# Optimization experiments

Hardware: AMD Instinct MI355X
Metric: run time of the kernel (lower is better)

Reference implementation:

```python
import jax, jax.numpy as jnp
import numpy as np

N, E, X_DIM, EA_DIM, HID, NL, NC, NGRAPH = 50000, 800000, 64, 16, 64, 3, 10, 64
BN_EPS = 1e-5
STD_EPS = 1e-5


def setup_inputs() -> dict:
    key = jax.random.key(0)
    ks = jax.random.split(key, 24)
    w = lambda k, sh: (jax.random.normal(k, sh, jnp.float32) * 0.05)
    inp = {
        'x': jax.random.normal(ks[0], (N, X_DIM), jnp.float32),
        'edge_index': jax.random.randint(ks[1], (2, E), 0, N),
        'batch': jnp.sort(jax.random.randint(ks[2], (N,), 0, NGRAPH)),
        'edge_attr': jax.random.normal(ks[3], (E, EA_DIM), jnp.float32),
        # node / edge encoders
        'node_w': w(ks[4], (X_DIM, HID)), 'node_b': jnp.zeros((HID,), jnp.float32),
        'edge_w': w(ks[5], (EA_DIM, HID)), 'edge_b': jnp.zeros((HID,), jnp.float32),
        # per-layer PNA post_nn Linear(12*3*HID -> HID) and BatchNorm
        'conv_w': w(ks[6], (NL, 12 * 3 * HID, HID)), 'conv_b': jnp.zeros((NL, HID), jnp.float32),
        'bn_g': jnp.ones((NL, HID), jnp.float32), 'bn_b': jnp.zeros((NL, HID), jnp.float32),
        # fc_out: HID -> HID/2 -> HID/4 -> NC
        'fc1_w': w(ks[7], (HID, HID // 2)), 'fc1_b': jnp.zeros((HID // 2,), jnp.float32),
        'fc2_w': w(ks[8], (HID // 2, HID // 4)), 'fc2_b': jnp.zeros((HID // 4,), jnp.float32),
        'fc3_w': w(ks[9], (HID // 4, NC)), 'fc3_b': jnp.zeros((NC,), jnp.float32),
    }
    return inp


def _pna_layer(x, src, dst, ea, deg, degc, log_deg, avg_log, w, b):
    # message: concat([x_i, x_j, edge_attr]) with x_i = x[dst], x_j = x[src]  -> [E, 3H]
    h = jnp.concatenate([x[dst], x[src], ea], axis=-1)
    inv = (1.0 / degc)[:, None]
    s1 = jax.ops.segment_sum(h, dst, num_segments=N)
    mean = s1 * inv
    mean_sq = jax.ops.segment_sum(h * h, dst, num_segments=N) * inv
    std = jnp.sqrt(jax.nn.relu(mean_sq - mean * mean) + STD_EPS)
    has = (deg > 0)[:, None]
    mx = jax.ops.segment_max(h, dst, num_segments=N)
    mx = jnp.where(has, mx, 0.0)
    mn = -jax.ops.segment_max(-h, dst, num_segments=N)
    mn = jnp.where(has, mn, 0.0)
    out = jnp.concatenate([mean, mn, mx, std], axis=-1)  # [N, 4*3H]
    amp = (log_deg / avg_log)[:, None]
    att = (avg_log / log_deg)[:, None]
    out = jnp.concatenate([out, out * amp, out * att], axis=-1)  # [N, 12*3H]
    return out @ w + b


def reference(x, edge_index, batch, edge_attr, node_w, node_b, edge_w, edge_b,
              conv_w, conv_b, bn_g, bn_b, fc1_w, fc1_b, fc2_w, fc2_b, fc3_w, fc3_b):
    src, dst = edge_index[0], edge_index[1]
    x = x @ node_w + node_b
    ea = edge_attr @ edge_w + edge_b
    deg = jax.ops.segment_sum(jnp.ones((E,), jnp.float32), dst, num_segments=N)
    degc = jnp.maximum(deg, 1.0)
    log_deg = jnp.log(degc + 1.0)
    # avg of log(deg+1) over nodes (equivalent to the histogram-based avg_deg['log'])
    avg_log = jnp.mean(jnp.log(deg + 1.0))
    for i in range(NL):
        h = _pna_layer(x, src, dst, ea, deg, degc, log_deg, avg_log, conv_w[i], conv_b[i])
        mu = jnp.mean(h, axis=0)
        var = jnp.mean((h - mu) ** 2, axis=0)  # biased var, as torch BN training mode
        h = (h - mu) * jax.lax.rsqrt(var + BN_EPS) * bn_g[i] + bn_b[i]
        x = jax.nn.relu(h) + x  # dropout is identity in eval
    # global mean pool over graphs
    gsum = jax.ops.segment_sum(x, batch, num_segments=NGRAPH)
    gcnt = jnp.maximum(jax.ops.segment_sum(jnp.ones((N,), jnp.float32), batch, num_segments=NGRAPH), 1.0)
    g = gsum / gcnt[:, None]
    g = jax.nn.relu(g @ fc1_w + fc1_b)
    g = jax.nn.relu(g @ fc2_w + fc2_b)
    return g @ fc3_w + fc3_b
```

## Files before the change

### kernel.cpp

```cpp
#include <hip/hip_runtime.h>
#include <math.h>

#define N_NODES 50000
#define N_EDGES 800000
#define NGRAPH  64
#define KEFF    576

typedef short bf16x8 __attribute__((ext_vector_type(8)));
typedef float f32x4  __attribute__((ext_vector_type(4)));
typedef float f32x16 __attribute__((ext_vector_type(16)));
typedef unsigned int u32;
typedef unsigned int u32x4 __attribute__((ext_vector_type(4)));

__device__ inline unsigned short f2bf_rne(float f) {
  unsigned u = __float_as_uint(f);
  unsigned r = u + 0x7FFFu + ((u >> 16) & 1u);
  return (unsigned short)(r >> 16);
}
__device__ inline float bf2f(unsigned short h) {
  return __uint_as_float(((unsigned)h) << 16);
}

__device__ inline u32 cvtpk_bf16(float a, float b) {
  u32 r;
  asm("v_cvt_pk_bf16_f32 %0, %1, %2" : "=v"(r) : "v"(a), "v"(b));
  return r;
}

__device__ inline void split2(float a, float b, u32& ph, u32& pl) {
  ph = cvtpk_bf16(a, b);
  float ha = __uint_as_float(ph << 16);
  float hb = __uint_as_float(ph & 0xFFFF0000u);
  pl = cvtpk_bf16(a - ha, b - hb);
}

__device__ inline bf16x8 pack_bf(u32 w0, u32 w1, u32 w2, u32 w3) {
  u32x4 t;
  t.x = w0; t.y = w1; t.z = w2; t.w = w3;
  return __builtin_bit_cast(bf16x8, t);
}


__global__ __launch_bounds__(256) void zero_kernel(
    int* __restrict__ cnt, float* __restrict__ gsum,
    double* __restrict__ bnacc, double* __restrict__ avgacc)
{
  int i = blockIdx.x * 256 + threadIdx.x;
  if (i < N_NODES) { cnt[i] = 0; return; }
  int j = i - N_NODES;
  if (j < NGRAPH * 64) { gsum[j] = 0.f; return; }
  int k = j - NGRAPH * 64;
  if (k < 3 * 128) { bnacc[k] = 0.0; return; }
  if (k == 3 * 128) *avgacc = 0.0;
}

__global__ __launch_bounds__(256) void node_enc_kernel(
    const float* __restrict__ xin, const float* __restrict__ nw,
    const float* __restrict__ nb, float* __restrict__ x)
{
  __shared__ float xs[256];
  int tid = threadIdx.x;
  int base = blockIdx.x * 256;
  xs[tid] = xin[base + tid];
  __syncthreads();
  int r = tid >> 6, j = tid & 63;
  float acc = nb[j];
#pragma unroll
  for (int t = 0; t < 64; t++) acc = fmaf(xs[r * 64 + t], nw[t * 64 + j], acc);
  x[base + tid] = acc;
}

__global__ void count_kernel(const int* __restrict__ dst, int* __restrict__ cnt,
                             int* __restrict__ rank)
{
  int e = blockIdx.x * 256 + threadIdx.x;
  rank[e] = atomicAdd(&cnt[dst[e]], 1);
}

__global__ __launch_bounds__(256) void scan_a_kernel(
    const int* __restrict__ cnt, int* __restrict__ bsum)
{
  __shared__ int s[256];
  int i = blockIdx.x * 256 + threadIdx.x;
  s[threadIdx.x] = (i < N_NODES) ? cnt[i] : 0;
  __syncthreads();
  for (int off = 128; off > 0; off >>= 1) {
    if (threadIdx.x < off) s[threadIdx.x] += s[threadIdx.x + off];
    __syncthreads();
  }
  if (threadIdx.x == 0) bsum[blockIdx.x] = s[0];
}

__global__ __launch_bounds__(256) void scan_b_kernel(
    const int* __restrict__ bsum, int* __restrict__ boff)
{
  __shared__ int s[256];
  int tid = threadIdx.x;
  int v = (tid < 196) ? bsum[tid] : 0;
  s[tid] = v;
  __syncthreads();
  for (int off = 1; off < 256; off <<= 1) {
    int t = (tid >= off) ? s[tid - off] : 0;
    __syncthreads();
    s[tid] += t;
    __syncthreads();
  }
  boff[tid] = s[tid] - v;
}

__global__ __launch_bounds__(256) void scan_c_kernel(
    const int* __restrict__ cnt, const int* __restrict__ boff,
    int* __restrict__ row_ptr)
{
  __shared__ int s[256];
  int tid = threadIdx.x;
  int i = blockIdx.x * 256 + tid;
  int v = (i < N_NODES) ? cnt[i] : 0;
  s[tid] = v;
  __syncthreads();
  for (int off = 1; off < 256; off <<= 1) {
    int t = (tid >= off) ? s[tid - off] : 0;
    __syncthreads();
    s[tid] += t;
    __syncthreads();
  }
  int incl = s[tid];
  int base = boff[blockIdx.x];
  if (i < N_NODES) row_ptr[i] = base + incl - v;
  if (i == N_NODES - 1) row_ptr[N_NODES] = base + incl;
}

__global__ void fill_kernel(const int* __restrict__ src, const int* __restrict__ dst,
                            const int* __restrict__ rank, const int* __restrict__ row_ptr,
                            int2* __restrict__ edata)
{
  int e = blockIdx.x * 256 + threadIdx.x;
  int d = dst[e];
  int pos = row_ptr[d] + rank[e];
  edata[pos] = make_int2(src[e], e);
}

__global__ __launch_bounds__(256) void deg_log_kernel(
    const int* __restrict__ cnt, float* __restrict__ log_deg,
    double* __restrict__ avgacc)
{
  __shared__ double sb[256];
  int i = blockIdx.x * 256 + threadIdx.x;
  double c = 0.0;
  if (i < N_NODES) {
    int d = cnt[i];
    int dc = d > 0 ? d : 1;
    log_deg[i] = logf((float)dc + 1.0f);
    c = (double)logf((float)d + 1.0f);
  }
  sb[threadIdx.x] = c;
  __syncthreads();
  for (int off = 128; off > 0; off >>= 1) {
    if (threadIdx.x < off) sb[threadIdx.x] += sb[threadIdx.x + off];
    __syncthreads();
  }
  if (threadIdx.x == 0) atomicAdd(avgacc, sb[0]);
}

__global__ void avg_gb_kernel(const double* __restrict__ avgacc,
                              float* __restrict__ avgf,
                              const int* __restrict__ batch,
                              int* __restrict__ gcnt)
{
  __shared__ int sb[65];
  int g = threadIdx.x;
  int lo = 0, hi = N_NODES;
  while (lo < hi) { int mid = (lo + hi) >> 1; if (batch[mid] < g) lo = mid + 1; else hi = mid; }
  sb[g] = lo;
  if (g == 0) { sb[64] = N_NODES; *avgf = (float)(*avgacc / (double)N_NODES); }
  __syncthreads();
  gcnt[g] = sb[g + 1] - sb[g];
}


__global__ __launch_bounds__(256) void wprep_kernel(
    const float* __restrict__ conv_w, unsigned short* __restrict__ wh,
    unsigned short* __restrict__ wl)
{
  int idx = blockIdx.x * 256 + threadIdx.x;
  int k = idx % 576;
  int c = (idx / 576) % 192;
  int l = idx / (576 * 192);
  int s = c >> 6, j = c & 63;
  const float* CW = conv_w + (size_t)l * 2304 * 64;
  float v;
  if (k < 64) {
    int base = s * 768 + k;
    v = CW[base * 64 + j] + CW[(base + 192) * 64 + j] + CW[(base + 384) * 64 + j];
  } else {
    const int srcseg[8] = {1, 2, 4, 5, 7, 8, 10, 11};
    int q = (k >> 6) - 1;
    int t = k & 63;
    v = CW[(s * 768 + srcseg[q] * 64 + t) * 64 + j];
  }
  unsigned short hh = f2bf_rne(v);
  size_t o = (((size_t)l * 12 + (c >> 4)) * 72 + (k >> 3)) * 128 + (c & 15) * 8 + (k & 7);
  wh[o] = hh;
  wl[o] = f2bf_rne(v - bf2f(hh));
}

__global__ void bprep_kernel(const float* __restrict__ conv_w, float* __restrict__ beff)
{
  int l = blockIdx.x;
  int s = threadIdx.x >> 6, j = threadIdx.x & 63;
  const float* CW = conv_w + (size_t)l * 2304 * 64 + (size_t)(s * 768 + 576) * 64;
  float sum = 0.f;
#pragma unroll
  for (int t = 0; t < 64; t++) sum += CW[t * 64 + j];
  beff[(l * 3 + s) * 64 + j] = sum * 0.0031622776601683794f;
}

__global__ __launch_bounds__(256) void ewprep_kernel(
    const float* __restrict__ edge_w, unsigned short* __restrict__ ewh,
    unsigned short* __restrict__ ewl)
{
  int tid = threadIdx.x;
#pragma unroll
  for (int it = 0; it < 4; it++) {
    int idx = tid + 256 * it;
    int j = idx & 7, cb = (idx >> 3) & 1, l31 = (idx >> 4) & 31, hf = idx >> 9;
    float v = edge_w[(hf * 8 + j) * 64 + cb * 32 + l31];
    unsigned short h = f2bf_rne(v);
    ewh[idx] = h;
    ewl[idx] = f2bf_rne(v - bf2f(h));
  }
}


#define AGG_E_BLOCKS 2048
#define AGG_E_WAVES  (AGG_E_BLOCKS * 4)

__global__ __launch_bounds__(256) void agg_e_kernel(
    const float* __restrict__ eattr,
    const unsigned short* __restrict__ ewh, const unsigned short* __restrict__ ewl,
    const float* __restrict__ edge_b, const int* __restrict__ row_ptr,
    const int2* __restrict__ edata,
    unsigned short* __restrict__ agg_h, unsigned short* __restrict__ agg_l)
{
  int lane = threadIdx.x & 63;
  int l31 = lane & 31, hf = lane >> 5;
  float eb = edge_b[lane];

  int fbase = (hf * 32 + l31) * 16;
  bf16x8 wbh[2], wbl[2];
#pragma unroll
  for (int cb = 0; cb < 2; cb++) {
    wbh[cb] = *(const bf16x8*)(ewh + fbase + cb * 8);
    wbl[cb] = *(const bf16x8*)(ewl + fbase + cb * 8);
  }

  const f32x16 zero = {};
  int wid = __builtin_amdgcn_readfirstlane(blockIdx.x * 4 + (threadIdx.x >> 6));

  auto process = [&](int n, int s0, int s1, float4 d0, float4 d1) {
    int deg = s1 - s0;
    float se[2] = {0.f, 0.f}, sq[2] = {0.f, 0.f};
    float mx[2] = {-3.4e38f, -3.4e38f}, mn[2] = {3.4e38f, 3.4e38f};
    if (deg > 0) {
      int j = s0;
      while (true) {
        int remh = (s1 - j) - 4 * hf;
        u32 h0, l0, h1, l1, h2, l2, h3, l3;
        split2(d0.x, d0.y, h0, l0); split2(d0.z, d0.w, h1, l1);
        split2(d1.x, d1.y, h2, l2); split2(d1.z, d1.w, h3, l3);
        bf16x8 ahi = pack_bf(h0, h1, h2, h3), alo = pack_bf(l0, l1, l2, l3);
#pragma unroll
        for (int cb = 0; cb < 2; cb++) {
          f32x16 acc = __builtin_amdgcn_mfma_f32_32x32x16_bf16(ahi, wbh[cb], zero, 0, 0, 0);
          acc = __builtin_amdgcn_mfma_f32_32x32x16_bf16(alo, wbh[cb], acc, 0, 0, 0);
          acc = __builtin_amdgcn_mfma_f32_32x32x16_bf16(ahi, wbl[cb], acc, 0, 0, 0);
#pragma unroll
          for (int reg = 0; reg < 16; reg++) {
            const int baserow = (reg & 3) + 8 * (reg >> 2);
            float v = acc[reg];
            float vm = (baserow < remh) ? v : 0.f;
            se[cb] += vm; sq[cb] = fmaf(vm, vm, sq[cb]);
            mx[cb] = fmaxf(mx[cb], v); mn[cb] = fminf(mn[cb], v);
          }
        }
        j += 32;
        if (j >= s1) break;
        int id = edata[min(j + l31, s1 - 1)].y;
        const float4* pp = (const float4*)(eattr + (size_t)id * 16 + hf * 8);
        d0 = pp[0]; d1 = pp[1];
      }
    }
#pragma unroll
    for (int cb = 0; cb < 2; cb++) {
      se[cb] += __shfl_xor(se[cb], 32, 64);
      sq[cb] += __shfl_xor(sq[cb], 32, 64);
      mx[cb] = fmaxf(mx[cb], __shfl_xor(mx[cb], 32, 64));
      mn[cb] = fminf(mn[cb], __shfl_xor(mn[cb], 32, 64));
    }
    float SE = hf ? se[1] : se[0];
    float SQ = hf ? sq[1] : sq[0];
    float MX = hf ? mx[1] : mx[0];
    float MN = hf ? mn[1] : mn[0];

    float inv = 1.0f / fmaxf((float)deg, 1.0f);
    bool has = deg > 0;
    float m0 = SE * inv, ms0 = SQ * inv;
    float sd_e = sqrtf(fmaxf(ms0 - m0 * m0, 0.f) + 1e-5f);
    float m_e = has ? m0 + eb : 0.f;
    float mx_e = has ? MX + eb : 0.f;
    float mn_e = has ? MN + eb : 0.f;

    unsigned short* bh = agg_h + (size_t)n * KEFF;
    unsigned short* bl = agg_l + (size_t)n * KEFF;
#define W2(off, val) { float _v = (val); unsigned short _h = f2bf_rne(_v); \
                       bh[(off) + lane] = _h; bl[(off) + lane] = f2bf_rne(_v - bf2f(_h)); }
    W2(128, m_e); W2(256, mn_e); W2(384, mx_e); W2(512, sd_e);
#undef W2
  };

  for (int p = wid; p < N_NODES / 2; p += AGG_E_WAVES) {
    int nA = 2 * p;
    int r0 = row_ptr[nA], r1 = row_ptr[nA + 1], r2 = row_ptr[nA + 2];
    int idA = 0, idB = 0;
    if (r1 > r0) idA = edata[min(r0 + l31, r1 - 1)].y;
    if (r2 > r1) idB = edata[min(r1 + l31, r2 - 1)].y;
    float4 da0 = {}, da1 = {}, db0 = {}, db1 = {};
    if (r1 > r0) {
      const float4* pa = (const float4*)(eattr + (size_t)idA * 16 + hf * 8);
      da0 = pa[0]; da1 = pa[1];
    }
    if (r2 > r1) {
      const float4* pb = (const float4*)(eattr + (size_t)idB * 16 + hf * 8);
      db0 = pb[0]; db1 = pb[1];
    }
    process(nA, r0, r1, da0, da1);
    process(nA + 1, r1, r2, db0, db1);
  }
}


__global__ __launch_bounds__(256) void agg_x_kernel(
    const float* __restrict__ x, const int2* __restrict__ edata,
    const int* __restrict__ row_ptr,
    unsigned short* __restrict__ agg_h, unsigned short* __restrict__ agg_l)
{
  int lane = threadIdx.x & 63;
  int n = blockIdx.x * 4 + (threadIdx.x >> 6);
  if (n >= N_NODES) return;
  float xd = x[(size_t)n * 64 + lane];
  int s0 = row_ptr[n], s1 = row_ptr[n + 1];
  float sA = 0.f, sB = 0.f, sC = 0.f, sD = 0.f;
  float qA = 0.f, qB = 0.f, qC = 0.f, qD = 0.f;
  float mx0 = -3.4e38f, mx1 = -3.4e38f, mn0 = 3.4e38f, mn1 = 3.4e38f;
  int j = s0;
  for (; j + 7 < s1; j += 8) {
    int e0 = edata[j].x,     e1 = edata[j + 1].x, e2 = edata[j + 2].x, e3 = edata[j + 3].x;
    int e4 = edata[j + 4].x, e5 = edata[j + 5].x, e6 = edata[j + 6].x, e7 = edata[j + 7].x;
    float x0 = x[(size_t)e0 * 64 + lane];
    float x1 = x[(size_t)e1 * 64 + lane];
    float x2 = x[(size_t)e2 * 64 + lane];
    float x3 = x[(size_t)e3 * 64 + lane];
    float x4 = x[(size_t)e4 * 64 + lane];
    float x5 = x[(size_t)e5 * 64 + lane];
    float x6 = x[(size_t)e6 * 64 + lane];
    float x7 = x[(size_t)e7 * 64 + lane];
    sA += x0; sB += x1; sC += x2; sD += x3;
    sA += x4; sB += x5; sC += x6; sD += x7;
    qA = fmaf(x0, x0, qA); qB = fmaf(x1, x1, qB);
    qC = fmaf(x2, x2, qC); qD = fmaf(x3, x3, qD);
    qA = fmaf(x4, x4, qA); qB = fmaf(x5, x5, qB);
    qC = fmaf(x6, x6, qC); qD = fmaf(x7, x7, qD);
    mx0 = fmaxf(mx0, fmaxf(fmaxf(x0, x1), fmaxf(x2, x3)));
    mx1 = fmaxf(mx1, fmaxf(fmaxf(x4, x5), fmaxf(x6, x7)));
    mn0 = fminf(mn0, fminf(fminf(x0, x1), fminf(x2, x3)));
    mn1 = fminf(mn1, fminf(fminf(x4, x5), fminf(x6, x7)));
  }
  if (j < s1) {
    int last = s1 - 1;
    int rem = s1 - j;
    int e0 = edata[j].x;
    int e1 = edata[j + 1 < s1 ? j + 1 : last].x;
    int e2 = edata[j + 2 < s1 ? j + 2 : last].x;
    int e3 = edata[j + 3 < s1 ? j + 3 : last].x;
    int e4 = edata[j + 4 < s1 ? j + 4 : last].x;
    int e5 = edata[j + 5 < s1 ? j + 5 : last].x;
    int e6 = edata[j + 6 < s1 ? j + 6 : last].x;
    int e7 = edata[j + 7 < s1 ? j + 7 : last].x;
    float x0 = x[(size_t)e0 * 64 + lane];
    float x1 = x[(size_t)e1 * 64 + lane];
    float x2 = x[(size_t)e2 * 64 + lane];
    float x3 = x[(size_t)e3 * 64 + lane];
    float x4 = x[(size_t)e4 * 64 + lane];
    float x5 = x[(size_t)e5 * 64 + lane];
    float x6 = x[(size_t)e6 * 64 + lane];
    float x7 = x[(size_t)e7 * 64 + lane];
    mx0 = fmaxf(mx0, fmaxf(fmaxf(x0, x1), fmaxf(x2, x3)));
    mx1 = fmaxf(mx1, fmaxf(fmaxf(x4, x5), fmaxf(x6, x7)));
    mn0 = fminf(mn0, fminf(fminf(x0, x1), fminf(x2, x3)));
    mn1 = fminf(mn1, fminf(fminf(x4, x5), fminf(x6, x7)));
    float z1 = 1 < rem ? x1 : 0.f;
    float z2 = 2 < rem ? x2 : 0.f;
    float z3 = 3 < rem ? x3 : 0.f;
    float z4 = 4 < rem ? x4 : 0.f;
    float z5 = 5 < rem ? x5 : 0.f;
    float z6 = 6 < rem ? x6 : 0.f;
    float z7 = 7 < rem ? x7 : 0.f;
    sA += x0; sB += z1; sC += z2; sD += z3;
    sA += z4; sB += z5; sC += z6; sD += z7;
    qA = fmaf(x0, x0, qA); qB = fmaf(z1, z1, qB);
    qC = fmaf(z2, z2, qC); qD = fmaf(z3, z3, qD);
    qA = fmaf(z4, z4, qA); qB = fmaf(z5, z5, qB);
    qC = fmaf(z6, z6, qC); qD = fmaf(z7, z7, qD);
  }
  float sx = (sA + sB) + (sC + sD);
  float qx = (qA + qB) + (qC + qD);
  float mxx = fmaxf(mx0, mx1), mnx = fminf(mn0, mn1);

  int deg = s1 - s0;
  float inv = 1.0f / fmaxf((float)deg, 1.0f);
  bool has = deg > 0;
  float m_s = sx * inv, ms_s = qx * inv;
  float sd_s = sqrtf(fmaxf(ms_s - m_s * m_s, 0.f) + 1e-5f);
  float mx_s = has ? mxx : 0.f, mn_s = has ? mnx : 0.f;

  unsigned short* bh = agg_h + (size_t)n * KEFF;
  unsigned short* bl = agg_l + (size_t)n * KEFF;
#define W2(off, val) { float _v = (val); unsigned short _h = f2bf_rne(_v); \
                       bh[(off) + lane] = _h; bl[(off) + lane] = f2bf_rne(_v - bf2f(_h)); }
  W2(0,   has ? xd : 0.f);
  W2(64,  m_s); W2(192, mn_s); W2(320, mx_s); W2(448, sd_s);
#undef W2
}


__global__ __launch_bounds__(256, 3) void gemm_kernel(
    const unsigned short* __restrict__ Ah, const unsigned short* __restrict__ Al,
    const unsigned short* __restrict__ Wh, const unsigned short* __restrict__ Wl,
    const float* __restrict__ beff, const float* __restrict__ bias,
    const float* __restrict__ log_deg, const float* __restrict__ avg_ptr,
    float* __restrict__ h, double* __restrict__ bnacc)
{
  __shared__ __align__(16) short AsH[64 * 40], AsL[64 * 40];
  int tid = threadIdx.x;
  int lane = tid & 63, w = tid >> 6;
  int quad = lane >> 4, l15 = lane & 15;
  int n0 = blockIdx.x * 64;

  int arow = tid >> 2, ac = tid & 3;
  int an = n0 + arow; if (an >= N_NODES) an = N_NODES - 1;
  const unsigned short* gah = Ah + (size_t)an * KEFF + ac * 8;
  const unsigned short* gal = Al + (size_t)an * KEFF + ac * 8;

  const unsigned short* pbh[3];
  const unsigned short* pbl[3];
#pragma unroll
  for (int s = 0; s < 3; s++) {
    size_t cb = (size_t)(s * 4 + w) * 72 * 128 + l15 * 8;
    pbh[s] = Wh + cb;
    pbl[s] = Wl + cb;
  }

  f32x4 acc[4][3] = {};
  float4 rh = *(const float4*)(gah);
  float4 rl = *(const float4*)(gal);

  for (int k0 = 0; k0 < KEFF; k0 += 32) {
    int koff = ((k0 >> 3) + quad) * 128;
    bf16x8 bhf[3], blf[3];
#pragma unroll
    for (int s = 0; s < 3; s++) {
      bhf[s] = *(const bf16x8*)(pbh[s] + koff);
      blf[s] = *(const bf16x8*)(pbl[s] + koff);
    }
    *(float4*)(AsH + arow * 40 + ac * 8) = rh;
    *(float4*)(AsL + arow * 40 + ac * 8) = rl;
    if (k0 + 32 < KEFF) {
      rh = *(const float4*)(gah + k0 + 32);
      rl = *(const float4*)(gal + k0 + 32);
    }
    __syncthreads();

#pragma unroll
    for (int i = 0; i < 4; i++) {
      int row = i * 16 + l15;
      bf16x8 ah = *(const bf16x8*)(AsH + row * 40 + quad * 8);
      bf16x8 al = *(const bf16x8*)(AsL + row * 40 + quad * 8);
#pragma unroll
      for (int s = 0; s < 3; s++) {
        acc[i][s] = __builtin_amdgcn_mfma_f32_16x16x32_bf16(ah, bhf[s], acc[i][s], 0, 0, 0);
        acc[i][s] = __builtin_amdgcn_mfma_f32_16x16x32_bf16(al, bhf[s], acc[i][s], 0, 0, 0);
        acc[i][s] = __builtin_amdgcn_mfma_f32_16x16x32_bf16(ah, blf[s], acc[i][s], 0, 0, 0);
      }
    }
    __syncthreads();
  }

  float avg = *avg_ptr;
  int col = w * 16 + l15;
  float be0 = beff[col], be1 = beff[64 + col], be2 = beff[128 + col];
  float bi = bias[col];
  float ss = 0.f, sq = 0.f;
#pragma unroll
  for (int i = 0; i < 4; i++) {
#pragma unroll
    for (int r = 0; r < 4; r++) {
      int n = n0 + i * 16 + quad * 4 + r;
      if (n < N_NODES) {
        float ld = log_deg[n];
        float amp = ld / avg, att = avg / ld;
        float v = (acc[i][0][r] + be0) + amp * (acc[i][1][r] + be1)
                + att * (acc[i][2][r] + be2) + bi;
        h[(size_t)n * 64 + col] = v;
        ss += v; sq = fmaf(v, v, sq);
      }
    }
  }
  ss += __shfl_xor(ss, 16, 64); ss += __shfl_xor(ss, 32, 64);
  sq += __shfl_xor(sq, 16, 64); sq += __shfl_xor(sq, 32, 64);
  if (quad == 0) {
    atomicAdd(&bnacc[col], (double)ss);
    atomicAdd(&bnacc[64 + col], (double)sq);
  }
}


__global__ __launch_bounds__(256) void apply_kernel(
    const float* __restrict__ h, const double* __restrict__ acc,
    const float* __restrict__ g, const float* __restrict__ bnb,
    float* __restrict__ x)
{
  __shared__ float smu[64], ssc[64];
  int tid = threadIdx.x;
  if (tid < 64) {
    double mu = acc[tid] / (double)N_NODES;
    double var = acc[64 + tid] / (double)N_NODES - mu * mu;
    double rstd = 1.0 / sqrt(var + 1e-5);
    smu[tid] = (float)mu;
    ssc[tid] = (float)(rstd * (double)g[tid]);
  }
  __syncthreads();
  int i4 = blockIdx.x * 256 + tid;
  const float4* h4 = (const float4*)h;
  float4* x4 = (float4*)x;
  int c4 = (i4 & 15) * 4;
  float4 hv = h4[i4], xv = x4[i4];
  float4 bb = ((const float4*)bnb)[i4 & 15];
  float4 r;
  r.x = fmaxf((hv.x - smu[c4])     * ssc[c4]     + bb.x, 0.f) + xv.x;
  r.y = fmaxf((hv.y - smu[c4 + 1]) * ssc[c4 + 1] + bb.y, 0.f) + xv.y;
  r.z = fmaxf((hv.z - smu[c4 + 2]) * ssc[c4 + 2] + bb.z, 0.f) + xv.z;
  r.w = fmaxf((hv.w - smu[c4 + 3]) * ssc[c4 + 3] + bb.w, 0.f) + xv.w;
  x4[i4] = r;
}


__global__ __launch_bounds__(256) void pool_kernel(
    const float* __restrict__ x, const int* __restrict__ batch,
    float* __restrict__ gsum)
{
  int tid = threadIdx.x;
  int j = tid & 63, ri = tid >> 6;
  float acc = 0.f; int cur = -1;
  for (int k = 0; k < 16; k++) {
    int n = blockIdx.x * 64 + k * 4 + ri;
    if (n < N_NODES) {
      int b = batch[n];
      if (b != cur) {
        if (cur >= 0) atomicAdd(&gsum[cur * 64 + j], acc);
        cur = b; acc = 0.f;
      }
      acc += x[(size_t)n * 64 + j];
    }
  }
  if (cur >= 0) atomicAdd(&gsum[cur * 64 + j], acc);
}

__global__ __launch_bounds__(64) void fc_kernel(
    const float* __restrict__ gsum, const int* __restrict__ gcnt,
    const float* __restrict__ w1, const float* __restrict__ b1,
    const float* __restrict__ w2, const float* __restrict__ b2,
    const float* __restrict__ w3, const float* __restrict__ b3,
    float* __restrict__ out)
{
  __shared__ float w1s[64 * 32], w2s[32 * 16], w3s[16 * 10];
  __shared__ float b1s[32], b2s[16], b3s[10];
  __shared__ float gvs[64], a1s[32], a2s[16];
  int g = blockIdx.x, tid = threadIdx.x;

#pragma unroll
  for (int i = 0; i < 32; i++) w1s[tid + 64 * i] = w1[tid + 64 * i];
#pragma unroll
  for (int i = 0; i < 8; i++)  w2s[tid + 64 * i] = w2[tid + 64 * i];
  { int i2 = tid; if (i2 < 160) w3s[i2] = w3[i2];
    i2 = tid + 64; if (i2 < 160) w3s[i2] = w3[i2];
    i2 = tid + 128; if (i2 < 160) w3s[i2] = w3[i2]; }
  if (tid < 32) b1s[tid] = b1[tid];
  if (tid < 16) b2s[tid] = b2[tid];
  if (tid < 10) b3s[tid] = b3[tid];
  float cnt = fmaxf((float)gcnt[g], 1.0f);
  gvs[tid] = gsum[g * 64 + tid] / cnt;
  __syncthreads();

  {
    int o = tid & 31, half = tid >> 5;
    float s = 0.f;
#pragma unroll
    for (int j = 0; j < 32; j++)
      s = fmaf(gvs[half * 32 + j], w1s[(half * 32 + j) * 32 + o], s);
    s += __shfl_xor(s, 32, 64);
    if (half == 0) a1s[o] = fmaxf(s + b1s[o], 0.f);
  }
  __syncthreads();

  {
    int o = tid & 15, part = tid >> 4;
    float s = 0.f;
#pragma unroll
    for (int j = 0; j < 8; j++)
      s = fmaf(a1s[part * 8 + j], w2s[(part * 8 + j) * 16 + o], s);
    s += __shfl_xor(s, 16, 64);
    s += __shfl_xor(s, 32, 64);
    if (part == 0) a2s[o] = fmaxf(s + b2s[o], 0.f);
  }
  __syncthreads();

  if (tid < 10) {
    float s = b3s[tid];
#pragma unroll
    for (int j = 0; j < 16; j++) s = fmaf(a2s[j], w3s[j * 10 + tid], s);
    out[g * 10 + tid] = s;
  }
}


extern "C" void kernel_launch(void* const* d_in, const int* in_sizes, int n_in,
                              void* d_out, int out_size, void* d_ws, size_t ws_size,
                              hipStream_t stream)
{
  (void)in_sizes; (void)n_in; (void)out_size; (void)ws_size;
  const float* xin    = (const float*)d_in[0];
  const int*   ei     = (const int*)d_in[1];
  const int*   batch  = (const int*)d_in[2];
  const float* eattr  = (const float*)d_in[3];
  const float* node_w = (const float*)d_in[4];
  const float* node_b = (const float*)d_in[5];
  const float* edge_w = (const float*)d_in[6];
  const float* edge_b = (const float*)d_in[7];
  const float* conv_w = (const float*)d_in[8];
  const float* conv_b = (const float*)d_in[9];
  const float* bn_g   = (const float*)d_in[10];
  const float* bn_b   = (const float*)d_in[11];
  const float* fc1_w  = (const float*)d_in[12];
  const float* fc1_b  = (const float*)d_in[13];
  const float* fc2_w  = (const float*)d_in[14];
  const float* fc2_b  = (const float*)d_in[15];
  const float* fc3_w  = (const float*)d_in[16];
  const float* fc3_b  = (const float*)d_in[17];
  float* out = (float*)d_out;
  const int* srcp = ei;
  const int* dstp = ei + N_EDGES;

  char* p = (char*)d_ws;
  auto alloc = [&](size_t b) { char* r = p; p += (b + 255) & ~(size_t)255; return (void*)r; };
  float*  x       = (float*)alloc((size_t)N_NODES * 64 * 4);
  float*  h       = (float*)alloc((size_t)N_NODES * 64 * 4);
  unsigned short* agg_h = (unsigned short*)alloc((size_t)N_NODES * KEFF * 2);
  unsigned short* agg_l = (unsigned short*)alloc((size_t)N_NODES * KEFF * 2);
  unsigned short* wh    = (unsigned short*)alloc((size_t)3 * 12 * 72 * 128 * 2);
  unsigned short* wl    = (unsigned short*)alloc((size_t)3 * 12 * 72 * 128 * 2);
  int2*   edata   = (int2*)alloc((size_t)N_EDGES * 8);
  int*    rank    = (int*)alloc((size_t)N_EDGES * 4);
  float*  beff    = (float*)alloc((size_t)3 * 3 * 64 * 4);
  int*    row_ptr = (int*)alloc((N_NODES + 1) * 4);
  int*    cnt     = (int*)alloc((size_t)N_NODES * 4);
  float*  log_deg = (float*)alloc((size_t)N_NODES * 4);
  int*    bsum    = (int*)alloc(256 * 4);
  int*    boff    = (int*)alloc(256 * 4);
  double* avgacc  = (double*)alloc(256);
  float*  avgf    = (float*)alloc(256);
  double* bnacc   = (double*)alloc(3 * 128 * 8);
  float*  gsum    = (float*)alloc((size_t)NGRAPH * 64 * 4);
  int*    gcnt    = (int*)alloc((size_t)NGRAPH * 4);
  unsigned short* ewh = (unsigned short*)alloc(1024 * 2);
  unsigned short* ewl = (unsigned short*)alloc(1024 * 2);

  zero_kernel<<<213, 256, 0, stream>>>(cnt, gsum, bnacc, avgacc);
  node_enc_kernel<<<12500, 256, 0, stream>>>(xin, node_w, node_b, x);
  count_kernel<<<3125, 256, 0, stream>>>(dstp, cnt, rank);
  scan_a_kernel<<<196, 256, 0, stream>>>(cnt, bsum);
  scan_b_kernel<<<1, 256, 0, stream>>>(bsum, boff);
  scan_c_kernel<<<196, 256, 0, stream>>>(cnt, boff, row_ptr);
  fill_kernel<<<3125, 256, 0, stream>>>(srcp, dstp, rank, row_ptr, edata);
  deg_log_kernel<<<196, 256, 0, stream>>>(cnt, log_deg, avgacc);
  avg_gb_kernel<<<1, 64, 0, stream>>>(avgacc, avgf, batch, gcnt);
  wprep_kernel<<<1296, 256, 0, stream>>>(conv_w, wh, wl);
  bprep_kernel<<<3, 192, 0, stream>>>(conv_w, beff);
  ewprep_kernel<<<1, 256, 0, stream>>>(edge_w, ewh, ewl);

  agg_e_kernel<<<AGG_E_BLOCKS, 256, 0, stream>>>(eattr, ewh, ewl, edge_b,
                                                 row_ptr, edata, agg_h, agg_l);

  for (int l = 0; l < 3; l++) {
    agg_x_kernel<<<12500, 256, 0, stream>>>(x, edata, row_ptr, agg_h, agg_l);
    gemm_kernel<<<782, 256, 0, stream>>>(agg_h, agg_l,
                                         wh + (size_t)l * 12 * 72 * 128,
                                         wl + (size_t)l * 12 * 72 * 128,
                                         beff + l * 192, conv_b + l * 64,
                                         log_deg, avgf, h, bnacc + l * 128);
    apply_kernel<<<3125, 256, 0, stream>>>(h, bnacc + l * 128, bn_g + l * 64,
                                           bn_b + l * 64, x);
  }

  pool_kernel<<<782, 256, 0, stream>>>(x, batch, gsum);
  fc_kernel<<<NGRAPH, 64, 0, stream>>>(gsum, gcnt, fc1_w, fc1_b, fc2_w, fc2_b,
                                       fc3_w, fc3_b, out);
}
```

Measured before the change: 591.9 us.

## Fuse prep kernels and read x_i directly in GEMM instead of staging

Merges the degree/log computation into the first scan pass and combines the three weight-prep kernels into one launch, cutting several small kernel launches. It also stops agg_x from writing the self-feature x_i segment (hi/lo bf16) into the aggregate buffer; the GEMM instead loads x directly, masks it by degree, and splits it to bf16 hi/lo on the fly for the first two K-tiles. This removes a write and re-read of that segment per layer, at the cost of extra conversion work inside the GEMM prologue. The split2 helper is assumed to exist in the hidden part of the file.

```diff
diff --git a/kernel.cpp b/kernel.cpp
--- a/kernel.cpp
+++ b/kernel.cpp
@@ -77,18 +77,29 @@
   rank[e] = atomicAdd(&cnt[dst[e]], 1);
 }
 
-__global__ __launch_bounds__(256) void scan_a_kernel(
-    const int* __restrict__ cnt, int* __restrict__ bsum)
+__global__ __launch_bounds__(256) void scan_deg_kernel(
+    const int* __restrict__ cnt, int* __restrict__ bsum,
+    float* __restrict__ log_deg, double* __restrict__ avgacc)
 {
   __shared__ int s[256];
-  int i = blockIdx.x * 256 + threadIdx.x;
-  s[threadIdx.x] = (i < N_NODES) ? cnt[i] : 0;
+  __shared__ double sb[256];
+  int tid = threadIdx.x;
+  int i = blockIdx.x * 256 + tid;
+  int v = (i < N_NODES) ? cnt[i] : 0;
+  s[tid] = v;
+  double c = 0.0;
+  if (i < N_NODES) {
+    int dc = v > 0 ? v : 1;
+    log_deg[i] = logf((float)dc + 1.0f);
+    c = (double)logf((float)v + 1.0f);
+  }
+  sb[tid] = c;
   __syncthreads();
   for (int off = 128; off > 0; off >>= 1) {
-    if (threadIdx.x < off) s[threadIdx.x] += s[threadIdx.x + off];
+    if (tid < off) { s[tid] += s[tid + off]; sb[tid] += sb[tid + off]; }
     __syncthreads();
   }
-  if (threadIdx.x == 0) bsum[blockIdx.x] = s[0];
+  if (tid == 0) { bsum[blockIdx.x] = s[0]; atomicAdd(avgacc, sb[0]); }
 }
 
 __global__ __launch_bounds__(256) void scan_b_kernel(
@@ -138,28 +149,6 @@
   int d = dst[e];
   int pos = row_ptr[d] + rank[e];
   edata[pos] = make_int2(src[e], e);
-}
-
-__global__ __launch_bounds__(256) void deg_log_kernel(
-    const int* __restrict__ cnt, float* __restrict__ log_deg,
-    double* __restrict__ avgacc)
-{
-  __shared__ double sb[256];
-  int i = blockIdx.x * 256 + threadIdx.x;
-  double c = 0.0;
-  if (i < N_NODES) {
-    int d = cnt[i];
-    int dc = d > 0 ? d : 1;
-    log_deg[i] = logf((float)dc + 1.0f);
-    c = (double)logf((float)d + 1.0f);
-  }
-  sb[threadIdx.x] = c;
-  __syncthreads();
-  for (int off = 128; off > 0; off >>= 1) {
-    if (threadIdx.x < off) sb[threadIdx.x] += sb[threadIdx.x + off];
-    __syncthreads();
-  }
-  if (threadIdx.x == 0) atomicAdd(avgacc, sb[0]);
 }
 
 __global__ void avg_gb_kernel(const double* __restrict__ avgacc,
@@ -178,56 +167,56 @@
 }
 
 
-__global__ __launch_bounds__(256) void wprep_kernel(
-    const float* __restrict__ conv_w, unsigned short* __restrict__ wh,
-    unsigned short* __restrict__ wl)
-{
-  int idx = blockIdx.x * 256 + threadIdx.x;
-  int k = idx % 576;
-  int c = (idx / 576) % 192;
-  int l = idx / (576 * 192);
-  int s = c >> 6, j = c & 63;
-  const float* CW = conv_w + (size_t)l * 2304 * 64;
-  float v;
-  if (k < 64) {
-    int base = s * 768 + k;
-    v = CW[base * 64 + j] + CW[(base + 192) * 64 + j] + CW[(base + 384) * 64 + j];
+__global__ __launch_bounds__(256) void prep_kernel(
+    const float* __restrict__ conv_w, const float* __restrict__ edge_w,
+    unsigned short* __restrict__ wh, unsigned short* __restrict__ wl,
+    float* __restrict__ beff,
+    unsigned short* __restrict__ ewh, unsigned short* __restrict__ ewl)
+{
+  int b = blockIdx.x, tid = threadIdx.x;
+  if (b < 1296) {
+    int idx = b * 256 + tid;
+    int k = idx % 576;
+    int c = (idx / 576) % 192;
+    int l = idx / (576 * 192);
+    int s = c >> 6, j = c & 63;
+    const float* CW = conv_w + (size_t)l * 2304 * 64;
+    float v;
+    if (k < 64) {
+      int base = s * 768 + k;
+      v = CW[base * 64 + j] + CW[(base + 192) * 64 + j] + CW[(base + 384) * 64 + j];
+    } else {
+      const int srcseg[8] = {1, 2, 4, 5, 7, 8, 10, 11};
+      int q = (k >> 6) - 1;
+      int t = k & 63;
+      v = CW[(s * 768 + srcseg[q] * 64 + t) * 64 + j];
+    }
+    unsigned short hh = f2bf_rne(v);
+    size_t o = (((size_t)l * 12 + (c >> 4)) * 72 + (k >> 3)) * 128 + (c & 15) * 8 + (k & 7);
+    wh[o] = hh;
+    wl[o] = f2bf_rne(v - bf2f(hh));
+  } else if (b == 1296) {
+    if (tid < 192) {
+      int s = tid >> 6, j = tid & 63;
+#pragma unroll
+      for (int l = 0; l < 3; l++) {
+        const float* CW = conv_w + (size_t)l * 2304 * 64 + (size_t)(s * 768 + 576) * 64;
+        float sum = 0.f;
+#pragma unroll
+        for (int t = 0; t < 64; t++) sum += CW[t * 64 + j];
+        beff[(l * 3 + s) * 64 + j] = sum * 0.0031622776601683794f;
+      }
+    }
   } else {
-    const int srcseg[8] = {1, 2, 4, 5, 7, 8, 10, 11};
-    int q = (k >> 6) - 1;
-    int t = k & 63;
-    v = CW[(s * 768 + srcseg[q] * 64 + t) * 64 + j];
-  }
-  unsigned short hh = f2bf_rne(v);
-  size_t o = (((size_t)l * 12 + (c >> 4)) * 72 + (k >> 3)) * 128 + (c & 15) * 8 + (k & 7);
-  wh[o] = hh;
-  wl[o] = f2bf_rne(v - bf2f(hh));
-}
-
-__global__ void bprep_kernel(const float* __restrict__ conv_w, float* __restrict__ beff)
-{
-  int l = blockIdx.x;
-  int s = threadIdx.x >> 6, j = threadIdx.x & 63;
-  const float* CW = conv_w + (size_t)l * 2304 * 64 + (size_t)(s * 768 + 576) * 64;
-  float sum = 0.f;
-#pragma unroll
-  for (int t = 0; t < 64; t++) sum += CW[t * 64 + j];
-  beff[(l * 3 + s) * 64 + j] = sum * 0.0031622776601683794f;
-}
-
-__global__ __launch_bounds__(256) void ewprep_kernel(
-    const float* __restrict__ edge_w, unsigned short* __restrict__ ewh,
-    unsigned short* __restrict__ ewl)
-{
-  int tid = threadIdx.x;
-#pragma unroll
-  for (int it = 0; it < 4; it++) {
-    int idx = tid + 256 * it;
-    int j = idx & 7, cb = (idx >> 3) & 1, l31 = (idx >> 4) & 31, hf = idx >> 9;
-    float v = edge_w[(hf * 8 + j) * 64 + cb * 32 + l31];
-    unsigned short h = f2bf_rne(v);
-    ewh[idx] = h;
-    ewl[idx] = f2bf_rne(v - bf2f(h));
+#pragma unroll
+    for (int it = 0; it < 4; it++) {
+      int idx = tid + 256 * it;
+      int j = idx & 7, cb = (idx >> 3) & 1, l31 = (idx >> 4) & 31, hf = idx >> 9;
+      float v = edge_w[(hf * 8 + j) * 64 + cb * 32 + l31];
+      unsigned short h = f2bf_rne(v);
+      ewh[idx] = h;
+      ewl[idx] = f2bf_rne(v - bf2f(h));
+    }
   }
 }
 
@@ -347,7 +336,6 @@
   int lane = threadIdx.x & 63;
   int n = blockIdx.x * 4 + (threadIdx.x >> 6);
   if (n >= N_NODES) return;
-  float xd = x[(size_t)n * 64 + lane];
   int s0 = row_ptr[n], s1 = row_ptr[n + 1];
   float sA = 0.f, sB = 0.f, sC = 0.f, sD = 0.f;
   float qA = 0.f, qB = 0.f, qC = 0.f, qD = 0.f;
@@ -427,13 +415,13 @@
   unsigned short* bl = agg_l + (size_t)n * KEFF;
 #define W2(off, val) { float _v = (val); unsigned short _h = f2bf_rne(_v); \
                        bh[(off) + lane] = _h; bl[(off) + lane] = f2bf_rne(_v - bf2f(_h)); }
-  W2(0,   has ? xd : 0.f);
   W2(64,  m_s); W2(192, mn_s); W2(320, mx_s); W2(448, sd_s);
 #undef W2
 }
 
 
 __global__ __launch_bounds__(256, 3) void gemm_kernel(
+    const float* __restrict__ x, const int* __restrict__ cnt,
     const unsigned short* __restrict__ Ah, const unsigned short* __restrict__ Al,
     const unsigned short* __restrict__ Wh, const unsigned short* __restrict__ Wl,
     const float* __restrict__ beff, const float* __restrict__ bias,
@@ -448,6 +436,8 @@
 
   int arow = tid >> 2, ac = tid & 3;
   int an = n0 + arow; if (an >= N_NODES) an = N_NODES - 1;
+  const float* gx = x + (size_t)an * 64 + ac * 8;
+  float xm = (cnt[an] > 0) ? 1.f : 0.f;
   const unsigned short* gah = Ah + (size_t)an * KEFF + ac * 8;
   const unsigned short* gal = Al + (size_t)an * KEFF + ac * 8;
 
@@ -461,8 +451,23 @@
   }
 
   f32x4 acc[4][3] = {};
-  float4 rh = *(const float4*)(gah);
-  float4 rl = *(const float4*)(gal);
+
+  auto packx = [&](int k0, float4& rh, float4& rl) {
+    float4 a = *(const float4*)(gx + k0);
+    float4 b = *(const float4*)(gx + k0 + 4);
+    u32 h0, l0, h1, l1, h2, l2, h3, l3;
+    split2(a.x * xm, a.y * xm, h0, l0);
+    split2(a.z * xm, a.w * xm, h1, l1);
+    split2(b.x * xm, b.y * xm, h2, l2);
+    split2(b.z * xm, b.w * xm, h3, l3);
+    u32x4 th; th.x = h0; th.y = h1; th.z = h2; th.w = h3;
+    u32x4 tl; tl.x = l0; tl.y = l1; tl.z = l2; tl.w = l3;
+    rh = __builtin_bit_cast(float4, th);
+    rl = __builtin_bit_cast(float4, tl);
+  };
+
+  float4 rh, rl;
+  packx(0, rh, rl);
 
   for (int k0 = 0; k0 < KEFF; k0 += 32) {
     int koff = ((k0 >> 3) + quad) * 128;
@@ -475,8 +480,12 @@
     *(float4*)(AsH + arow * 40 + ac * 8) = rh;
     *(float4*)(AsL + arow * 40 + ac * 8) = rl;
     if (k0 + 32 < KEFF) {
-      rh = *(const float4*)(gah + k0 + 32);
-      rl = *(const float4*)(gal + k0 + 32);
+      if (k0 == 0) {
+        packx(32, rh, rl);
+      } else {
+        rh = *(const float4*)(gah + k0 + 32);
+        rl = *(const float4*)(gal + k0 + 32);
+      }
     }
     __syncthreads();
 
@@ -687,22 +696,19 @@
   zero_kernel<<<213, 256, 0, stream>>>(cnt, gsum, bnacc, avgacc);
   node_enc_kernel<<<12500, 256, 0, stream>>>(xin, node_w, node_b, x);
   count_kernel<<<3125, 256, 0, stream>>>(dstp, cnt, rank);
-  scan_a_kernel<<<196, 256, 0, stream>>>(cnt, bsum);
+  scan_deg_kernel<<<196, 256, 0, stream>>>(cnt, bsum, log_deg, avgacc);
   scan_b_kernel<<<1, 256, 0, stream>>>(bsum, boff);
   scan_c_kernel<<<196, 256, 0, stream>>>(cnt, boff, row_ptr);
   fill_kernel<<<3125, 256, 0, stream>>>(srcp, dstp, rank, row_ptr, edata);
-  deg_log_kernel<<<196, 256, 0, stream>>>(cnt, log_deg, avgacc);
   avg_gb_kernel<<<1, 64, 0, stream>>>(avgacc, avgf, batch, gcnt);
-  wprep_kernel<<<1296, 256, 0, stream>>>(conv_w, wh, wl);
-  bprep_kernel<<<3, 192, 0, stream>>>(conv_w, beff);
-  ewprep_kernel<<<1, 256, 0, stream>>>(edge_w, ewh, ewl);
+  prep_kernel<<<1298, 256, 0, stream>>>(conv_w, edge_w, wh, wl, beff, ewh, ewl);
 
   agg_e_kernel<<<AGG_E_BLOCKS, 256, 0, stream>>>(eattr, ewh, ewl, edge_b,
                                                  row_ptr, edata, agg_h, agg_l);
 
   for (int l = 0; l < 3; l++) {
     agg_x_kernel<<<12500, 256, 0, stream>>>(x, edata, row_ptr, agg_h, agg_l);
-    gemm_kernel<<<782, 256, 0, stream>>>(agg_h, agg_l,
+    gemm_kernel<<<782, 256, 0, stream>>>(x, cnt, agg_h, agg_l,
                                          wh + (size_t)l * 12 * 72 * 128,
                                          wl + (size_t)l * 12 * 72 * 128,
                                          beff + l * 192, conv_b + l * 64,
```

Result: slower. 619.8 us (+4.7%).
